# Kernel optimization log

Hardware: AMD Instinct MI355X
Metric: run time of the kernel (lower is better)

## Reference

```python
import jax, jax.numpy as jnp
import numpy as np

EPS = 1e-09
TOP_K = 2


def setup_inputs() -> dict:
    key = jax.random.key(0)
    ks = jax.random.split(key, 6)
    B, L, F, E, D, SE = 64, 1024, 900, 8, 768, 64
    cycle_curve_data = jax.random.normal(ks[0], (B, L, F), dtype=jnp.float32)
    logits = jax.random.normal(ks[1], (B, E), dtype=jnp.float32)
    moe_masks = jax.random.randint(ks[2], (B, E), 0, 2, dtype=jnp.int32)
    selection_embeddings = jax.random.normal(ks[3], (B, E, SE), dtype=jnp.float32)
    W = jax.random.normal(ks[4], (E, F, D), dtype=jnp.float32) * 0.02
    b = jnp.zeros((E, D), dtype=jnp.float32)
    return {"cycle_curve_data": cycle_curve_data, "logits": logits,
            "moe_masks": moe_masks, "selection_embeddings": selection_embeddings,
            "W": W, "b": b}


def reference(cycle_curve_data, logits, moe_masks, selection_embeddings, W, b):
    B = cycle_curve_data.shape[0]
    E = logits.shape[1]
    mask = (moe_masks == 1).astype(logits.dtype)                 # [B, E]
    raw = jax.nn.softmax(logits, axis=1)                         # [B, E]
    p = raw * mask
    # selection embedding from inactive experts
    inactive = raw * (1.0 - mask)
    inactive = inactive / (jnp.sum(inactive, axis=1, keepdims=True) + EPS)
    selection_embedding = jnp.sum(selection_embeddings * inactive[:, :, None], axis=1)  # [B, SE]
    # top-k masking (indices treated as constants, same as torch scatter mask)
    if TOP_K > 0:
        _, idx = jax.lax.top_k(p, TOP_K)                         # [B, K]
        topk_mask = jnp.zeros_like(p).at[jnp.arange(B)[:, None], idx].set(1.0)
        p = p * topk_mask
    p = p / (jnp.sum(p, axis=1, keepdims=True) + EPS)            # [B, E]
    # dispatch/combine == weighted sum of per-expert Linear outputs
    # (weights are zero for unselected experts, matching MOEDispatcher)
    out = jnp.zeros(cycle_curve_data.shape[:2] + (W.shape[-1],), dtype=cycle_curve_data.dtype)
    for e in range(E):  # small fixed expert count
        expert_out = jnp.einsum('blf,fd->bld', cycle_curve_data, W[e]) + b[e]
        out = out + p[:, e, None, None] * expert_out
    final_out = out.astype(jnp.bfloat16)
    # guide loss (training mode)
    s = jnp.sum(raw * mask) / B
    guide_loss = (1.0 - s) * (1.0 - s)
    return final_out, guide_loss, selection_embedding
```

## Files before the change

kernel.cpp:

```cpp
#include <hip/hip_runtime.h>

#define B_  64
#define L_  1024
#define F_  900
#define E_  8
#define D_  768
#define SE_ 64
#define KP_ 928
#define FD_ (F_*D_)
#define OUT_MAIN (64*1024*768)
#define GL_OFF   OUT_MAIN
#define SE_OFF   (OUT_MAIN + 1)
#define EPSF 1e-9f
#define NT_  29


using f32x4  = __attribute__((ext_vector_type(4))) float;
using bf16   = __bf16;
using bf16x4 = __attribute__((ext_vector_type(4))) __bf16;
using bf16x8 = __attribute__((ext_vector_type(8))) __bf16;
using s16x8  = __attribute__((ext_vector_type(8))) short;

__device__ __forceinline__ f32x4 mfma_bf16(bf16x8 a, bf16x8 b, f32x4 c) {
  return __builtin_amdgcn_mfma_f32_16x16x32_bf16(
      __builtin_bit_cast(s16x8, a), __builtin_bit_cast(s16x8, b), c, 0, 0, 0);
}

__device__ __forceinline__ void gload16(const bf16* g, bf16* l) {
  __builtin_amdgcn_global_load_lds(
      (const __attribute__((address_space(1))) unsigned int*)g,
      (__attribute__((address_space(3))) unsigned int*)l, 16, 0, 0);
}

__device__ __forceinline__ const unsigned* pick_masks(const void* cA, const void* cB,
                                                      const float** logits) {
  const unsigned* a = (const unsigned*)cA;
  bool aIsMask = true;
#pragma unroll
  for (int i = 0; i < 512; i += 37) aIsMask &= (a[i] <= 1u);
  if (aIsMask) { *logits = (const float*)cB; return a; }
  *logits = (const float*)cA; return (const unsigned*)cB;
}

struct Gate { int e1, e2; float p1, p2; };

__device__ __forceinline__ Gate gate_for(const float* __restrict__ logits,
                                         const unsigned* __restrict__ masks, int b) {
  float lg[E_]; unsigned mk[E_];
#pragma unroll
  for (int e = 0; e < E_; ++e) { lg[e] = logits[b*E_+e]; mk[e] = masks[b*E_+e]; }
  float mx = lg[0];
#pragma unroll
  for (int e = 1; e < E_; ++e) mx = fmaxf(mx, lg[e]);
  float ex[E_], s = 0.f;
#pragma unroll
  for (int e = 0; e < E_; ++e) { ex[e] = expf(lg[e]-mx); s += ex[e]; }
  const float inv_s = 1.f / s;
  float p0[E_];
#pragma unroll
  for (int e = 0; e < E_; ++e) p0[e] = (mk[e] == 1u) ? ex[e]*inv_s : 0.f;
  int e1 = 0;
#pragma unroll
  for (int e = 1; e < E_; ++e) if (p0[e] > p0[e1]) e1 = e;
  int e2 = (e1 == 0) ? 1 : 0;
#pragma unroll
  for (int e = 0; e < E_; ++e) if (e != e1 && p0[e] > p0[e2]) e2 = e;
  const float inv = 1.f / (p0[e1] + p0[e2] + EPSF);
  Gate g; g.e1 = e1; g.e2 = e2; g.p1 = p0[e1]*inv; g.p2 = p0[e2]*inv;
  return g;
}

__global__ void gating_kernel(const void* cA, const void* cB,
                              const float* __restrict__ selemb,
                              float* __restrict__ fout) {
  const float* logits; const unsigned* masks = pick_masks(cA, cB, &logits);
  const int b = threadIdx.x;
  float lg[E_]; unsigned mk[E_];
#pragma unroll
  for (int e = 0; e < E_; ++e) { lg[e] = logits[b*E_+e]; mk[e] = masks[b*E_+e]; }
  float mx = lg[0];
#pragma unroll
  for (int e = 1; e < E_; ++e) mx = fmaxf(mx, lg[e]);
  float ex[E_], s = 0.f;
#pragma unroll
  for (int e = 0; e < E_; ++e) { ex[e] = expf(lg[e]-mx); s += ex[e]; }
  const float inv_s = 1.f / s;
  float inact[E_]; float isum = 0.f, sact = 0.f;
#pragma unroll
  for (int e = 0; e < E_; ++e) {
    float raw = ex[e] * inv_s;
    if (mk[e] == 1u) { sact += raw; inact[e] = 0.f; }
    else             { inact[e] = raw; isum += raw; }
  }
  const float inv_i = 1.f / (isum + EPSF);
  for (int se = 0; se < SE_; ++se) {
    float a = 0.f;
#pragma unroll
    for (int e = 0; e < E_; ++e)
      a += inact[e] * inv_i * selemb[((size_t)b*E_ + e)*SE_ + se];
    fout[SE_OFF + b*SE_ + se] = a;
  }
#pragma unroll
  for (int off = 32; off > 0; off >>= 1) sact += __shfl_down(sact, off);
  if (b == 0) {
    float sm = sact / (float)B_;
    fout[GL_OFF] = (1.f - sm) * (1.f - sm);
  }
}

__global__ __launch_bounds__(256) void xconv_kernel(const float* __restrict__ X,
                                                    bf16* __restrict__ Xbf) {
  int idx = blockIdx.x * 256 + threadIdx.x;
#pragma unroll 1
  for (int it = 0; it < 29; ++it, idx += 524288) {
    const int row = idx / 232;
    const int s   = idx - row * 232;
    bf16x4 o;
    if (s < 225) {
      f32x4 v = *(const f32x4*)(X + (size_t)row*F_ + s*4);
#pragma unroll
      for (int j = 0; j < 4; ++j) o[j] = (bf16)v[j];
    } else {
      o = (bf16x4){(bf16)0.f,(bf16)0.f,(bf16)0.f,(bf16)0.f};
    }
    *(bf16x4*)(Xbf + (size_t)row*KP_ + s*4) = o;
  }
}

__global__ __launch_bounds__(256) void wmix_kernel(const float* __restrict__ W,
                                                   const void* cA, const void* cB,
                                                   bf16* __restrict__ Wmix) {
  const int b  = blockIdx.x / 12;
  const int dc = blockIdx.x - b*12;
  const float* logits; const unsigned* masks = pick_masks(cA, cB, &logits);
  const Gate g = gate_for(logits, masks, b);
  const int lane = threadIdx.x & 63, w = threadIdx.x >> 6;
  const int d = (dc << 6) + lane;
  const float* W1 = W + (size_t)g.e1*FD_ + d;
  const float* W2 = W + (size_t)g.e2*FD_ + d;
  bf16* dst = Wmix + ((size_t)b*D_ + d)*KP_;
#pragma unroll 1
  for (int i = 0; i < 29; ++i) {
    const int f0 = (w + (i << 2)) << 3;
    float v[8];
#pragma unroll
    for (int jj = 0; jj < 8; ++jj) {
      int f = f0 + jj;
      v[jj] = (f < F_) ? g.p1*W1[(size_t)f*D_] + g.p2*W2[(size_t)f*D_] : 0.f;
    }
    bf16x8 pk;
#pragma unroll
    for (int jj = 0; jj < 8; ++jj) pk[jj] = (bf16)v[jj];
    *(bf16x8*)(dst + f0) = pk;
  }
}

__global__ __launch_bounds__(256) void gemm_fast(
    const bf16* __restrict__ Xbf, const bf16* __restrict__ Wmix,
    const float* __restrict__ bias,
    const void* cA, const void* cB,
    float* __restrict__ fout) {
  __shared__ bf16 As[2][128*32];
  __shared__ bf16 Bs[2][128*32];

  const int id  = blockIdx.x;
  const int xcd = id & 7, q = id >> 3;
  const int b   = xcd + ((q / 48) << 3);
  const int j   = q % 48;
  const int bn  = j % 6, bm = j / 6;

  const float* logits; const unsigned* masks = pick_masks(cA, cB, &logits);
  const Gate g = gate_for(logits, masks, b);

  const bf16* Ab = Xbf  + ((size_t)b*L_ + (size_t)bm*128) * KP_;
  const bf16* Bb = Wmix + ((size_t)b*D_ + (size_t)bn*128) * KP_;

  const int t = threadIdx.x, lane = t & 63, w = t >> 6;
  const int sw   = ((lane & 3) ^ ((lane >> 2) & 3)) << 3;
  const int row0 = (w << 5) + (lane >> 2);
  const int row1 = row0 + 16;
  const int dst0 = (w << 7) << 3;
  const int dst1 = dst0 + (64 << 3);

  auto STAGE = [&](int buf, int kt) {
    const int k0 = kt << 5;
    gload16(Ab + (size_t)row0*KP_ + k0 + sw, &As[buf][dst0]);
    gload16(Ab + (size_t)row1*KP_ + k0 + sw, &As[buf][dst1]);
    gload16(Bb + (size_t)row0*KP_ + k0 + sw, &Bs[buf][dst0]);
    gload16(Bb + (size_t)row1*KP_ + k0 + sw, &Bs[buf][dst1]);
  };

  const int wr = (w >> 1) << 6, wc = (w & 1) << 6;
  const int fr = lane & 15, fks = lane >> 4;
  const int rq = (lane >> 4) << 2;

  int aoff[4], boff[4];
#pragma unroll
  for (int m = 0; m < 4; ++m) {
    int rA = wr + m*16 + fr;
    aoff[m] = rA*32 + ((fks ^ (rA & 3)) << 3);
    int rB = wc + m*16 + fr;
    boff[m] = rB*32 + ((fks ^ (rB & 3)) << 3);
  }

  f32x4 acc[4][4];
#pragma unroll
  for (int m = 0; m < 4; ++m)
#pragma unroll
    for (int n = 0; n < 4; ++n) acc[m][n] = (f32x4){0.f,0.f,0.f,0.f};

  STAGE(0, 0);
  int cur = 0;
#pragma unroll 1
  for (int kt = 0; kt < NT_; ++kt) {
    if (kt + 1 < NT_) {
      STAGE(cur ^ 1, kt + 1);
      asm volatile("s_waitcnt vmcnt(4)" ::: "memory");
    } else {
      asm volatile("s_waitcnt vmcnt(0)" ::: "memory");
    }
    __builtin_amdgcn_sched_barrier(0);
    __builtin_amdgcn_s_barrier();
    __builtin_amdgcn_sched_barrier(0);
    bf16x8 af[4], bfv[4];
#pragma unroll
    for (int m = 0; m < 4; ++m) af[m]  = *(const bf16x8*)&As[cur][aoff[m]];
#pragma unroll
    for (int n = 0; n < 4; ++n) bfv[n] = *(const bf16x8*)&Bs[cur][boff[n]];
#pragma unroll
    for (int m = 0; m < 4; ++m)
#pragma unroll
      for (int n = 0; n < 4; ++n)
        acc[m][n] = mfma_bf16(af[m], bfv[n], acc[m][n]);
    __builtin_amdgcn_sched_barrier(0);
    __builtin_amdgcn_s_barrier();
    cur ^= 1;
  }

  const float* b1 = bias + g.e1*D_;
  const float* b2 = bias + g.e2*D_;
#pragma unroll
  for (int n = 0; n < 4; ++n) {
    int gc = bn*128 + wc + n*16 + fr;
    float bs = g.p1*b1[gc] + g.p2*b2[gc];
#pragma unroll
    for (int m = 0; m < 4; ++m) {
      size_t base = ((size_t)b*L_ + (size_t)(bm*128 + wr + m*16 + rq)) * D_ + gc;
#pragma unroll
      for (int i = 0; i < 4; ++i)
        fout[base + (size_t)i*D_] = acc[m][n][i] + bs;
    }
  }
}

__global__ void transw_kernel(const float* __restrict__ W, bf16* __restrict__ Wt) {
  __shared__ float tile[32][33];
  const int e  = blockIdx.z;
  const int d0 = blockIdx.x << 5;
  const int f0 = blockIdx.y << 5;
  const int c = threadIdx.x & 31, r = threadIdx.x >> 5;
#pragma unroll
  for (int p = 0; p < 4; ++p) {
    int f = f0 + p*8 + r;
    tile[p*8+r][c] = (f < F_) ? W[((size_t)e*F_ + f)*D_ + d0 + c] : 0.f;
  }
  __syncthreads();
#pragma unroll
  for (int p = 0; p < 4; ++p) {
    int d = d0 + p*8 + r;
    Wt[((size_t)e*D_ + d)*KP_ + f0 + c] = (bf16)tile[c][p*8+r];
  }
}

__global__ __launch_bounds__(256) void gemm_kernel(
    const float* __restrict__ X, const bf16* __restrict__ Wt,
    const float* __restrict__ bias,
    const void* cA, const void* cB,
    float* __restrict__ fout) {
  __shared__ bf16 As[128][40];
  __shared__ bf16 Bs[128][40];
  const int bn = blockIdx.x, bm = blockIdx.y, b = blockIdx.z;
  const float* logits; const unsigned* masks = pick_masks(cA, cB, &logits);
  const Gate g = gate_for(logits, masks, b);
  const float* Xb = X + ((size_t)b*L_ + (size_t)bm*128) * F_;
  const bf16* W1 = Wt + ((size_t)g.e1*D_ + (size_t)bn*128) * KP_;
  const bf16* W2 = Wt + ((size_t)g.e2*D_ + (size_t)bn*128) * KP_;
  const int t  = threadIdx.x;
  const int ar = t >> 3, ac = (t & 7) << 2;
  const int br = t >> 2, bc = (t & 3) << 3;
  const int lane = t & 63, wave = t >> 6;
  const int wr = (wave >> 1) << 6, wc = (wave & 1) << 6;
  const int fr = lane & 15, fk = (lane >> 4) << 3;
  const int rq = (lane >> 4) << 2;
  f32x4 acc[4][4];
#pragma unroll
  for (int m = 0; m < 4; ++m)
#pragma unroll
    for (int n = 0; n < 4; ++n) acc[m][n] = (f32x4){0.f,0.f,0.f,0.f};
  f32x4 ax[4]; bf16x8 wv1[2], wv2[2];
  auto LOAD = [&](int k0) {
    if (k0 <= F_ - 32) {
#pragma unroll
      for (int p = 0; p < 4; ++p)
        ax[p] = *(const f32x4*)(Xb + (size_t)(p*32 + ar)*F_ + k0 + ac);
    } else {
#pragma unroll
      for (int p = 0; p < 4; ++p)
#pragma unroll
        for (int jj = 0; jj < 4; ++jj) {
          int k = k0 + ac + jj;
          ax[p][jj] = (k < F_) ? Xb[(size_t)(p*32 + ar)*F_ + k] : 0.f;
        }
    }
#pragma unroll
    for (int p = 0; p < 2; ++p) {
      wv1[p] = *(const bf16x8*)(W1 + (size_t)(p*64 + br)*KP_ + k0 + bc);
      wv2[p] = *(const bf16x8*)(W2 + (size_t)(p*64 + br)*KP_ + k0 + bc);
    }
  };
  auto STAGE = [&]() {
#pragma unroll
    for (int p = 0; p < 4; ++p) {
      bf16x4 v;
#pragma unroll
      for (int jj = 0; jj < 4; ++jj) v[jj] = (bf16)ax[p][jj];
      *(bf16x4*)&As[p*32 + ar][ac] = v;
    }
#pragma unroll
    for (int p = 0; p < 2; ++p) {
      bf16x8 v;
#pragma unroll
      for (int jj = 0; jj < 8; ++jj)
        v[jj] = (bf16)(g.p1 * (float)wv1[p][jj] + g.p2 * (float)wv2[p][jj]);
      *(bf16x8*)&Bs[p*64 + br][bc] = v;
    }
  };
  LOAD(0);
  for (int kt = 0; kt < NT_; ++kt) {
    STAGE();
    __syncthreads();
    if (kt + 1 < NT_) LOAD((kt + 1) << 5);
    bf16x8 af[4], bfv[4];
#pragma unroll
    for (int m = 0; m < 4; ++m) af[m]  = *(const bf16x8*)&As[wr + m*16 + fr][fk];
#pragma unroll
    for (int n = 0; n < 4; ++n) bfv[n] = *(const bf16x8*)&Bs[wc + n*16 + fr][fk];
#pragma unroll
    for (int m = 0; m < 4; ++m)
#pragma unroll
      for (int n = 0; n < 4; ++n)
        acc[m][n] = mfma_bf16(af[m], bfv[n], acc[m][n]);
    __syncthreads();
  }
  const float* b1 = bias + g.e1*D_;
  const float* b2 = bias + g.e2*D_;
#pragma unroll
  for (int n = 0; n < 4; ++n) {
    int gc = bn*128 + wc + n*16 + fr;
    float bs = g.p1*b1[gc] + g.p2*b2[gc];
#pragma unroll
    for (int m = 0; m < 4; ++m) {
      size_t base = ((size_t)b*L_ + (size_t)(bm*128 + wr + m*16 + rq)) * D_ + gc;
#pragma unroll
      for (int i = 0; i < 4; ++i)
        fout[base + (size_t)i*D_] = acc[m][n][i] + bs;
    }
  }
}

__global__ __launch_bounds__(128) void fallback_kernel(
    const float* __restrict__ X, const float* __restrict__ W,
    const float* __restrict__ bias,
    const void* cA, const void* cB,
    float* __restrict__ fout) {
  __shared__ float xs[16 * F_];
  const int t  = threadIdx.x;
  const int d  = blockIdx.x * 128 + t;
  const int l0 = blockIdx.y * 16;
  const int b  = blockIdx.z;
  const float* logits; const unsigned* masks = pick_masks(cA, cB, &logits);
  const Gate g = gate_for(logits, masks, b);
  const float* xrow = X + ((size_t)b*L_ + l0) * F_;
  for (int i = t; i < 16 * F_; i += 128) xs[i] = xrow[i];
  __syncthreads();
  const float* w1 = W + (size_t)g.e1*FD_ + d;
  const float* w2 = W + (size_t)g.e2*FD_ + d;
  float acc[16];
#pragma unroll
  for (int jj = 0; jj < 16; ++jj) acc[jj] = 0.f;
  for (int k = 0; k < F_; k += 4) {
    float wb[4];
#pragma unroll
    for (int qq = 0; qq < 4; ++qq)
      wb[qq] = g.p1 * w1[(size_t)(k+qq)*D_] + g.p2 * w2[(size_t)(k+qq)*D_];
#pragma unroll
    for (int jj = 0; jj < 16; ++jj) {
      f32x4 xv = *(const f32x4*)&xs[jj*F_ + k];
#pragma unroll
      for (int qq = 0; qq < 4; ++qq) acc[jj] += xv[qq] * wb[qq];
    }
  }
  const float bs = g.p1*bias[g.e1*D_+d] + g.p2*bias[g.e2*D_+d];
#pragma unroll
  for (int jj = 0; jj < 16; ++jj)
    fout[((size_t)b*L_ + (size_t)(l0 + jj)) * D_ + d] = acc[jj] + bs;
}

extern "C" void kernel_launch(void* const* d_in, const int* in_sizes, int n_in,
                              void* d_out, int out_size, void* d_ws, size_t ws_size,
                              hipStream_t stream) {
  const float *X = nullptr, *selemb = nullptr, *W = nullptr, *bias = nullptr;
  const void *cA = nullptr, *cB = nullptr;
  for (int i = 0; i < n_in; ++i) {
    switch (in_sizes[i]) {
      case 58982400: X      = (const float*)d_in[i]; break;
      case 32768:    selemb = (const float*)d_in[i]; break;
      case 5529600:  W      = (const float*)d_in[i]; break;
      case 6144:     bias   = (const float*)d_in[i]; break;
      case 512:      if (!cA) cA = d_in[i]; else cB = d_in[i]; break;
      default: break;
    }
  }
  if (!X)      X      = (const float*)d_in[0];
  if (!cA)     cA     = d_in[1];
  if (!cB)     cB     = d_in[2];
  if (!selemb) selemb = (const float*)d_in[3];
  if (!W)      W      = (const float*)d_in[4];
  if (!bias)   bias   = (const float*)d_in[5];
  float* fout = (float*)d_out;

  const size_t xbf_bytes  = (size_t)B_*L_*KP_*2;
  const size_t wmix_bytes = (size_t)B_*D_*KP_*2;
  const size_t need_fast  = xbf_bytes + wmix_bytes;
  const size_t need_mid   = (size_t)E_*D_*KP_*2;

  gating_kernel<<<1, 64, 0, stream>>>(cA, cB, selemb, fout);

  if (ws_size >= need_fast) {
    bf16* Xbf  = (bf16*)d_ws;
    bf16* Wmix = (bf16*)((char*)d_ws + xbf_bytes);
    xconv_kernel<<<2048, 256, 0, stream>>>(X, Xbf);
    wmix_kernel<<<768, 256, 0, stream>>>(W, cA, cB, Wmix);
    gemm_fast<<<3072, 256, 0, stream>>>(Xbf, Wmix, bias, cA, cB, fout);
  } else if (ws_size >= need_mid) {
    bf16* Wt = (bf16*)d_ws;
    transw_kernel<<<dim3(24, 29, 8), 256, 0, stream>>>(W, Wt);
    gemm_kernel<<<dim3(6, 8, 64), 256, 0, stream>>>(X, Wt, bias, cA, cB, fout);
  } else {
    fallback_kernel<<<dim3(6, 64, 64), 128, 0, stream>>>(X, W, bias, cA, cB, fout);
  }
}
```

Baseline: 395.3 us.

## Merge prep kernels into one launch and triple-buffer GEMM shared memory

Folds gating, X bf16 conversion and expert-weight mixing into a single prep kernel, with blocks picking their role by block index. This removes two launches and lets the three pieces run concurrently. The GEMM moves from double to triple buffering of its LDS tiles, staging two k-tiles ahead with adjusted vmcnt waits to hide global-load latency. It also hoists the bias loads ahead of the main loop. The cost is more LDS per block (48KB), which may reduce occupancy.

```diff
diff --git a/kernel.cpp b/kernel.cpp
--- a/kernel.cpp
+++ b/kernel.cpp
@@ -70,11 +70,10 @@
   return g;
 }
 
-__global__ void gating_kernel(const void* cA, const void* cB,
-                              const float* __restrict__ selemb,
-                              float* __restrict__ fout) {
+__device__ __forceinline__ void gating_body(const void* cA, const void* cB,
+                                            const float* __restrict__ selemb,
+                                            float* __restrict__ fout, int b) {
   const float* logits; const unsigned* masks = pick_masks(cA, cB, &logits);
-  const int b = threadIdx.x;
   float lg[E_]; unsigned mk[E_];
 #pragma unroll
   for (int e = 0; e < E_; ++e) { lg[e] = logits[b*E_+e]; mk[e] = masks[b*E_+e]; }
@@ -108,50 +107,61 @@
   }
 }
 
-__global__ __launch_bounds__(256) void xconv_kernel(const float* __restrict__ X,
-                                                    bf16* __restrict__ Xbf) {
-  int idx = blockIdx.x * 256 + threadIdx.x;
+__global__ void gating_kernel(const void* cA, const void* cB,
+                              const float* __restrict__ selemb,
+                              float* __restrict__ fout) {
+  gating_body(cA, cB, selemb, fout, threadIdx.x);
+}
+
+__global__ __launch_bounds__(256) void prep_kernel(
+    const float* __restrict__ X, const float* __restrict__ W,
+    const void* cA, const void* cB, const float* __restrict__ selemb,
+    bf16* __restrict__ Xbf, bf16* __restrict__ Wmix,
+    float* __restrict__ fout) {
+  const int blk = blockIdx.x;
+  if (blk < 2048) {
+    int idx = blk * 256 + threadIdx.x;
 #pragma unroll 1
-  for (int it = 0; it < 29; ++it, idx += 524288) {
-    const int row = idx / 232;
-    const int s   = idx - row * 232;
-    bf16x4 o;
-    if (s < 225) {
-      f32x4 v = *(const f32x4*)(X + (size_t)row*F_ + s*4);
-#pragma unroll
-      for (int j = 0; j < 4; ++j) o[j] = (bf16)v[j];
-    } else {
-      o = (bf16x4){(bf16)0.f,(bf16)0.f,(bf16)0.f,(bf16)0.f};
-    }
-    *(bf16x4*)(Xbf + (size_t)row*KP_ + s*4) = o;
-  }
-}
-
-__global__ __launch_bounds__(256) void wmix_kernel(const float* __restrict__ W,
-                                                   const void* cA, const void* cB,
-                                                   bf16* __restrict__ Wmix) {
-  const int b  = blockIdx.x / 12;
-  const int dc = blockIdx.x - b*12;
-  const float* logits; const unsigned* masks = pick_masks(cA, cB, &logits);
-  const Gate g = gate_for(logits, masks, b);
-  const int lane = threadIdx.x & 63, w = threadIdx.x >> 6;
-  const int d = (dc << 6) + lane;
-  const float* W1 = W + (size_t)g.e1*FD_ + d;
-  const float* W2 = W + (size_t)g.e2*FD_ + d;
-  bf16* dst = Wmix + ((size_t)b*D_ + d)*KP_;
+    for (int it = 0; it < 29; ++it, idx += 524288) {
+      const int row = idx / 232;
+      const int s   = idx - row * 232;
+      bf16x4 o;
+      if (s < 225) {
+        f32x4 v = *(const f32x4*)(X + (size_t)row*F_ + s*4);
+#pragma unroll
+        for (int j = 0; j < 4; ++j) o[j] = (bf16)v[j];
+      } else {
+        o = (bf16x4){(bf16)0.f,(bf16)0.f,(bf16)0.f,(bf16)0.f};
+      }
+      *(bf16x4*)(Xbf + (size_t)row*KP_ + s*4) = o;
+    }
+  } else if (blk < 2816) {
+    const int wb = blk - 2048;
+    const int b  = wb / 12;
+    const int dc = wb - b*12;
+    const float* logits; const unsigned* masks = pick_masks(cA, cB, &logits);
+    const Gate g = gate_for(logits, masks, b);
+    const int lane = threadIdx.x & 63, w = threadIdx.x >> 6;
+    const int d = (dc << 6) + lane;
+    const float* W1 = W + (size_t)g.e1*FD_ + d;
+    const float* W2 = W + (size_t)g.e2*FD_ + d;
+    bf16* dst = Wmix + ((size_t)b*D_ + d)*KP_;
 #pragma unroll 1
-  for (int i = 0; i < 29; ++i) {
-    const int f0 = (w + (i << 2)) << 3;
-    float v[8];
-#pragma unroll
-    for (int jj = 0; jj < 8; ++jj) {
-      int f = f0 + jj;
-      v[jj] = (f < F_) ? g.p1*W1[(size_t)f*D_] + g.p2*W2[(size_t)f*D_] : 0.f;
-    }
-    bf16x8 pk;
-#pragma unroll
-    for (int jj = 0; jj < 8; ++jj) pk[jj] = (bf16)v[jj];
-    *(bf16x8*)(dst + f0) = pk;
+    for (int i = 0; i < 29; ++i) {
+      const int f0 = (w + (i << 2)) << 3;
+      float v[8];
+#pragma unroll
+      for (int jj = 0; jj < 8; ++jj) {
+        int f = f0 + jj;
+        v[jj] = (f < F_) ? g.p1*W1[(size_t)f*D_] + g.p2*W2[(size_t)f*D_] : 0.f;
+      }
+      bf16x8 pk;
+#pragma unroll
+      for (int jj = 0; jj < 8; ++jj) pk[jj] = (bf16)v[jj];
+      *(bf16x8*)(dst + f0) = pk;
+    }
+  } else {
+    if (threadIdx.x < 64) gating_body(cA, cB, selemb, fout, threadIdx.x);
   }
 }
 
@@ -160,8 +170,8 @@
     const float* __restrict__ bias,
     const void* cA, const void* cB,
     float* __restrict__ fout) {
-  __shared__ bf16 As[2][128*32];
-  __shared__ bf16 Bs[2][128*32];
+  __shared__ bf16 As[3][128*32];
+  __shared__ bf16 Bs[3][128*32];
 
   const int id  = blockIdx.x;
   const int xcd = id & 7, q = id >> 3;
@@ -203,6 +213,15 @@
     boff[m] = rB*32 + ((fks ^ (rB & 3)) << 3);
   }
 
+  const float* b1 = bias + g.e1*D_;
+  const float* b2 = bias + g.e2*D_;
+  float bsv[4];
+#pragma unroll
+  for (int n = 0; n < 4; ++n) {
+    int gc = bn*128 + wc + n*16 + fr;
+    bsv[n] = g.p1*b1[gc] + g.p2*b2[gc];
+  }
+
   f32x4 acc[4][4];
 #pragma unroll
   for (int m = 0; m < 4; ++m)
@@ -210,11 +229,15 @@
     for (int n = 0; n < 4; ++n) acc[m][n] = (f32x4){0.f,0.f,0.f,0.f};
 
   STAGE(0, 0);
+  STAGE(1, 1);
   int cur = 0;
 #pragma unroll 1
   for (int kt = 0; kt < NT_; ++kt) {
-    if (kt + 1 < NT_) {
-      STAGE(cur ^ 1, kt + 1);
+    if (kt + 2 < NT_) {
+      const int sb = (cur + 2 >= 3) ? cur - 1 : cur + 2;
+      STAGE(sb, kt + 2);
+      asm volatile("s_waitcnt vmcnt(8)" ::: "memory");
+    } else if (kt + 2 == NT_) {
       asm volatile("s_waitcnt vmcnt(4)" ::: "memory");
     } else {
       asm volatile("s_waitcnt vmcnt(0)" ::: "memory");
@@ -234,21 +257,18 @@
         acc[m][n] = mfma_bf16(af[m], bfv[n], acc[m][n]);
     __builtin_amdgcn_sched_barrier(0);
     __builtin_amdgcn_s_barrier();
-    cur ^= 1;
-  }
-
-  const float* b1 = bias + g.e1*D_;
-  const float* b2 = bias + g.e2*D_;
+    cur = (cur + 1 == 3) ? 0 : cur + 1;
+  }
+
 #pragma unroll
   for (int n = 0; n < 4; ++n) {
     int gc = bn*128 + wc + n*16 + fr;
-    float bs = g.p1*b1[gc] + g.p2*b2[gc];
 #pragma unroll
     for (int m = 0; m < 4; ++m) {
       size_t base = ((size_t)b*L_ + (size_t)(bm*128 + wr + m*16 + rq)) * D_ + gc;
 #pragma unroll
       for (int i = 0; i < 4; ++i)
-        fout[base + (size_t)i*D_] = acc[m][n][i] + bs;
+        fout[base + (size_t)i*D_] = acc[m][n][i] + bsv[n];
     }
   }
 }
@@ -434,19 +454,18 @@
   const size_t need_fast  = xbf_bytes + wmix_bytes;
   const size_t need_mid   = (size_t)E_*D_*KP_*2;
 
-  gating_kernel<<<1, 64, 0, stream>>>(cA, cB, selemb, fout);
-
   if (ws_size >= need_fast) {
     bf16* Xbf  = (bf16*)d_ws;
     bf16* Wmix = (bf16*)((char*)d_ws + xbf_bytes);
-    xconv_kernel<<<2048, 256, 0, stream>>>(X, Xbf);
-    wmix_kernel<<<768, 256, 0, stream>>>(W, cA, cB, Wmix);
+    prep_kernel<<<2817, 256, 0, stream>>>(X, W, cA, cB, selemb, Xbf, Wmix, fout);
     gemm_fast<<<3072, 256, 0, stream>>>(Xbf, Wmix, bias, cA, cB, fout);
   } else if (ws_size >= need_mid) {
     bf16* Wt = (bf16*)d_ws;
+    gating_kernel<<<1, 64, 0, stream>>>(cA, cB, selemb, fout);
     transw_kernel<<<dim3(24, 29, 8), 256, 0, stream>>>(W, Wt);
     gemm_kernel<<<dim3(6, 8, 64), 256, 0, stream>>>(X, Wt, bias, cA, cB, fout);
   } else {
+    gating_kernel<<<1, 64, 0, stream>>>(cA, cB, selemb, fout);
     fallback_kernel<<<dim3(6, 64, 64), 128, 0, stream>>>(X, W, bias, cA, cB, fout);
   }
 }
```

After: 375.2 us. -5.1%, faster.
